# Kernel tuning notes

Hardware: AMD Instinct MI355X
Metric: run time of the kernel (lower is better)

Reference implementation:

```python
import math
import jax, jax.numpy as jnp
import numpy as np

B, S, E, H = 4, 1024, 768, 12
HD = E // H
NUM_BUCKETS, MAX_DIST = 320, 800


def setup_inputs() -> dict:
    key = jax.random.key(0)
    ks = jax.random.split(key, 8)
    w = lambda k, sh: jax.random.normal(k, sh, jnp.float32) * 0.02
    return {
        "hidden_states": jax.random.normal(ks[0], (B, S, E), jnp.float32),
        "q_w": w(ks[1], (E, E)), "q_b": jnp.zeros((E,), jnp.float32),
        "k_w": w(ks[2], (E, E)), "k_b": jnp.zeros((E,), jnp.float32),
        "v_w": w(ks[3], (E, E)), "v_b": jnp.zeros((E,), jnp.float32),
        "out_w": w(ks[4], (E, E)), "out_b": jnp.zeros((E,), jnp.float32),
        "gru_const": jnp.ones((1, H, 1, 1), jnp.float32),
        "gru_w": w(ks[5], (8, HD)), "gru_b": jnp.zeros((8,), jnp.float32),
        "rel_embed": w(ks[6], (NUM_BUCKETS, H)),
    }


def _relative_positions_bucket(rel):
    # rel: (S, S) int32, rel = memory_pos - context_pos
    nb = NUM_BUCKETS // 2
    buckets = (rel > 0).astype(jnp.int32) * nb
    rel = jnp.abs(rel)
    max_exact = nb // 2
    is_small = rel < max_exact
    large = jnp.log(rel.astype(jnp.float32) / max_exact)
    large = large / math.log(MAX_DIST / max_exact) * (nb - max_exact)
    large = (max_exact + large).astype(jnp.int32)
    large = jnp.minimum(large, nb - 1)
    return buckets + jnp.where(is_small, rel, large)


def _compute_position_bias(rel_embed):
    pos = jnp.arange(S, dtype=jnp.int32)
    rel = pos[None, :] - pos[:, None]              # (S, S)
    bucket = _relative_positions_bucket(rel)       # (S, S) int32
    return rel_embed[bucket].transpose(2, 0, 1)    # (H, S, S)


def reference(hidden_states, q_w, q_b, k_w, k_b, v_w, v_b, out_w, out_b,
              gru_const, gru_w, gru_b, rel_embed):
    position_bias = _compute_position_bias(rel_embed)          # (H, S, S)

    # gated relative-position bias
    ghs = hidden_states.reshape(B, S, H, HD).transpose(0, 2, 1, 3)   # (B,H,S,HD)
    proj = jnp.einsum("bhsd,ed->bhse", ghs, gru_w) + gru_b           # (B,H,S,8)
    proj = proj.reshape(B, H, S, 2, 4).sum(-1)                       # (B,H,S,2)
    gates = jax.nn.sigmoid(proj)
    gate_a, gate_b = gates[..., 0:1], gates[..., 1:2]                # (B,H,S,1)
    gate = gate_a * (gate_b * gru_const - 1.0) + 2.0                 # (B,H,S,1)
    gated_bias = gate[..., None, :, 0][..., None] * 0  # placeholder removed below
    gated_bias = gate * position_bias[None]                          # (B,H,S,S)

    scaling = HD ** -0.5
    q = (hidden_states @ q_w.T + q_b).reshape(B, S, H, HD).transpose(0, 2, 1, 3) * scaling
    k = (hidden_states @ k_w.T + k_b).reshape(B, S, H, HD).transpose(0, 2, 1, 3)
    v = (hidden_states @ v_w.T + v_b).reshape(B, S, H, HD).transpose(0, 2, 1, 3)

    scores = jnp.einsum("bhqd,bhkd->bhqk", q, k) + gated_bias
    attn = jax.nn.softmax(scores, axis=-1)
    ctx = jnp.einsum("bhqk,bhkd->bhqd", attn, v)                     # (B,H,S,HD)
    ctx = ctx.transpose(0, 2, 1, 3).reshape(B, S, E)
    attn_output = ctx @ out_w.T + out_b
    return attn_output, position_bias
```

## Files before the change

### kernel.cpp

```cpp
#include <hip/hip_runtime.h>

typedef unsigned short u16;
typedef __attribute__((ext_vector_type(4))) unsigned short u16x4;
typedef __attribute__((ext_vector_type(8))) short s8v;
typedef __attribute__((ext_vector_type(4))) float f4v;

#define BB 4
#define SS 1024
#define EE 768
#define HH 12
#define DD 64

#define NHS (BB * SS * EE)
#define NW  (EE * EE)
#define LOG2E 1.4426950408889634f

static __device__ __forceinline__ u16 f2bf(float x){
  unsigned int u = __float_as_uint(x);
  u += 0x7fffu + ((u >> 16) & 1u);
  return (u16)(u >> 16);
}
static __device__ __forceinline__ unsigned cvt_pk_bf16(float lo, float hi){
  unsigned r;
  asm("v_cvt_pk_bf16_f32 %0, %1, %2" : "=v"(r) : "v"(lo), "v"(hi));
  return r;
}
static __device__ __forceinline__ void stage16(const u16* g, u16* l){
  __builtin_amdgcn_global_load_lds(
      (const __attribute__((address_space(1))) void*)g,
      (__attribute__((address_space(3))) void*)l, 16, 0, 0);
}

__global__ __launch_bounds__(256) void prep_kernel(const float* __restrict__ hs,
                                                   const float* __restrict__ qw,
                                                   const float* __restrict__ kw,
                                                   const float* __restrict__ vw,
                                                   const float* __restrict__ ow,
                                                   u16* __restrict__ dst,
                                                   const float* __restrict__ rel_embed,
                                                   float* __restrict__ tbl,
                                                   const float* __restrict__ gru_w,
                                                   const float* __restrict__ gru_b,
                                                   const float* __restrict__ gru_c,
                                                   float* __restrict__ gate){
  const int bid = blockIdx.x;
  if (bid < 2688){
    size_t e = ((size_t)bid * 256 + threadIdx.x) * 8;
    const float* src;
    if      (e < (size_t)NHS)            src = hs + e;
    else if (e < (size_t)NHS + NW)       src = qw + (e - NHS);
    else if (e < (size_t)NHS + 2 * NW)   src = kw + (e - NHS - NW);
    else if (e < (size_t)NHS + 3 * NW)   src = vw + (e - NHS - 2 * (size_t)NW);
    else                                 src = ow + (e - NHS - 3 * (size_t)NW);
    f4v v0 = *(const f4v*)src, v1 = *(const f4v*)(src + 4);
    s8v o;
    #pragma unroll
    for (int i = 0; i < 4; i++){ o[i] = (short)f2bf(v0[i]); o[4 + i] = (short)f2bf(v1[i]); }
    size_t row = e / EE;
    int k = (int)(e - row * EE);
    size_t d = row * EE + (size_t)(k ^ (((int)row & 7) << 3));
    *(s8v*)(dst + d) = o;
  } else if (bid < 2784){
    int id = (bid - 2688) * 256 + threadIdx.x;
    int h = id >> 11, r = id & 2047;
    float v = 0.f;
    if (r < 2047){
      int rel = r - 1023;
      int bucket = (rel > 0) ? 160 : 0;
      int a = rel < 0 ? -rel : rel;
      int idx;
      if (a < 80) idx = a;
      else {
        float t = logf((float)a / 80.0f);
        t = t / 2.302585092994046f * 80.0f;
        int lg = (int)(80.0f + t);
        idx = lg < 159 ? lg : 159;
      }
      v = rel_embed[(idx + bucket) * HH + h];
    }
    tbl[id] = v;
  } else {
    int wid = (bid - 2784) * 4 + (threadIdx.x >> 6);
    int lane = threadIdx.x & 63;
    int s = wid & (SS - 1);
    int bh = wid >> 10;
    int h = bh % HH, b = bh / HH;
    float x = hs[(size_t)(b * SS + s) * EE + h * DD + lane];
    float w0 = gru_w[lane] + gru_w[64 + lane] + gru_w[128 + lane] + gru_w[192 + lane];
    float w1 = gru_w[256 + lane] + gru_w[320 + lane] + gru_w[384 + lane] + gru_w[448 + lane];
    float y0 = x * w0, y1 = x * w1;
    #pragma unroll
    for (int off = 1; off < 64; off <<= 1){
      y0 += __shfl_xor(y0, off);
      y1 += __shfl_xor(y1, off);
    }
    if (lane == 0){
      float s0 = y0 + gru_b[0] + gru_b[1] + gru_b[2] + gru_b[3];
      float s1 = y1 + gru_b[4] + gru_b[5] + gru_b[6] + gru_b[7];
      float ga = 1.f / (1.f + __expf(-s0));
      float gb = 1.f / (1.f + __expf(-s1));
      gate[wid] = ga * (gb * gru_c[h] - 1.0f) + 2.0f;
    }
  }
}

template<int EP>
static __device__ __forceinline__ void gemm_body(const u16* __restrict__ A,
                                                 const u16* __restrict__ Bw,
                                                 const float* __restrict__ bias,
                                                 void* __restrict__ Cp,
                                                 float scale, int m0, int n0){
  __shared__ __align__(16) u16 a_s[128 * 64];
  __shared__ __align__(16) u16 b_s[128 * 64];
  const int t = threadIdx.x;
  const int wave = t >> 6, lane = t & 63;
  const int lr = lane & 15, lg = lane >> 4;
  const int wm = (wave >> 1) * 64, wn = (wave & 1) * 64;
  const int srow = lane >> 3;
  const int scol = (lane & 7) * 8;
  const int swz = (lr & 7) << 3;

  const f4v zero = {0.f, 0.f, 0.f, 0.f};
  f4v acc[4][4];
  #pragma unroll
  for (int i = 0; i < 4; i++)
    #pragma unroll
    for (int j = 0; j < 4; j++) acc[i][j] = zero;

  for (int k0 = 0; k0 < EE; k0 += 64){
    if (k0) __syncthreads();
    #pragma unroll
    for (int i = 0; i < 4; i++){
      const int chunk = i * 4 + wave;
      const int r = chunk * 8 + srow;
      stage16(A  + (size_t)(m0 + r) * EE + k0 + scol, &a_s[chunk * 512]);
      stage16(Bw + (size_t)(n0 + r) * EE + k0 + scol, &b_s[chunk * 512]);
    }
    __syncthreads();
    #pragma unroll
    for (int kk = 0; kk < 2; kk++){
      const int cbase = (kk * 32 + lg * 8) ^ swz;
      s8v af[4], bf[4];
      #pragma unroll
      for (int i = 0; i < 4; i++){
        af[i] = *(const s8v*)&a_s[(wm + i * 16 + lr) * 64 + cbase];
        bf[i] = *(const s8v*)&b_s[(wn + i * 16 + lr) * 64 + cbase];
      }
      #pragma unroll
      for (int i = 0; i < 4; i++)
        #pragma unroll
        for (int j = 0; j < 4; j++)
          acc[i][j] = __builtin_amdgcn_mfma_f32_16x16x32_bf16(af[i], bf[j], acc[i][j], 0, 0, 0);
    }
  }

  #pragma unroll
  for (int ii = 0; ii < 4; ii++){
    const int row0 = m0 + wm + ii * 16 + lg * 4;
    const int bb = row0 >> 10;
    const int s0 = row0 & (SS - 1);
    #pragma unroll
    for (int j = 0; j < 4; j++){
      const int col = n0 + wn + j * 16 + lr;
      const float bv = bias[col];
      if (EP == 0){
        const int h = col >> 6, dim = col & 63;
        const int bh = bb * HH + h;
        u16* dst = (u16*)Cp + ((size_t)((bh * 64 + (s0 >> 4)) * 2 + (dim >> 5))) * 512
                   + ((dim >> 3) & 3) * 128 + (s0 & 15) * 8 + (dim & 7);
        #pragma unroll
        for (int r = 0; r < 4; r++)
          dst[r * 8] = f2bf((acc[ii][j][r] + bv) * scale);
      } else if (EP == 2){
        const int h = col >> 6, dim = col & 63;
        const int bh = bb * HH + h;
        u16x4 pk;
        #pragma unroll
        for (int r = 0; r < 4; r++) pk[r] = f2bf(acc[ii][j][r] + bv);
        *(u16x4*)((u16*)Cp + ((size_t)(((bh * 16 + (s0 >> 6)) * 2 + ((s0 >> 5) & 1)) * 4 + (dim >> 4))) * 512
                  + ((s0 >> 3) & 3) * 128 + (dim & 15) * 8 + (s0 & 7)) = pk;
      } else {
        #pragma unroll
        for (int r = 0; r < 4; r++)
          ((float*)Cp)[(size_t)(row0 + r) * EE + col] = acc[ii][j][r] + bv;
      }
    }
  }
}

__global__ __launch_bounds__(256) void gemm_qkv(const u16* __restrict__ A,
                                                const u16* __restrict__ wqkv,
                                                const float* __restrict__ bq,
                                                const float* __restrict__ bk,
                                                const float* __restrict__ bv,
                                                u16* __restrict__ qo,
                                                u16* __restrict__ ko,
                                                u16* __restrict__ vo){
  const int z = blockIdx.z;
  if (z == 2)
    gemm_body<2>(A, wqkv + 2 * (size_t)NW, bv, vo, 1.0f, blockIdx.x * 128, blockIdx.y * 128);
  else
    gemm_body<0>(A, wqkv + (size_t)z * NW, z ? bk : bq, z ? ko : qo,
                 z ? 1.0f : 0.125f * LOG2E, blockIdx.x * 128, blockIdx.y * 128);
}

__global__ __launch_bounds__(256) void gemm_out(const u16* __restrict__ A,
                                                const u16* __restrict__ Bw,
                                                const float* __restrict__ bias,
                                                float* __restrict__ Cp){
  gemm_body<1>(A, Bw, bias, Cp, 1.0f, blockIdx.x * 128, blockIdx.y * 128);
}

__global__ __launch_bounds__(256) void attn_kernel(const u16* __restrict__ qpack,
                                                   const u16* __restrict__ kpack,
                                                   const u16* __restrict__ vpack,
                                                   const float* __restrict__ gate,
                                                   const float* __restrict__ tbl,
                                                   u16* __restrict__ ctx,
                                                   float* __restrict__ pb){
  __shared__ __align__(16) float tbl_s[2048];
  __shared__ __align__(16) u16 kv_s[2][8192];
  __shared__ __align__(16) u16 p_s[4][16][72];
  const int t = threadIdx.x, wave = t >> 6, lane = t & 63;
  const int lr = lane & 15, lg = lane >> 4;
  const int i = blockIdx.x;
  const int xcd = i & 7, slot = i >> 3;
  const int bhg = xcd * 6 + (slot >> 4);
  const int qb  = slot & 15;
  const int b = bhg / HH, h = bhg % HH;
  const int bh = bhg;
  const int q0w = qb * 64 + wave * 16;
  {
    const float* th = tbl + h * 2048 + t * 8;
    *(f4v*)&tbl_s[t * 8]     = *(const f4v*)th;
    *(f4v*)&tbl_s[t * 8 + 4] = *(const f4v*)(th + 4);
  }
  const u16* qp = qpack + ((size_t)(bh * 64 + qb * 4 + wave)) * 1024 + lane * 8;
  const s8v qf0 = *(const s8v*)qp;
  const s8v qf1 = *(const s8v*)(qp + 512);
  const float gt = gate[(size_t)bh * SS + q0w + lr] * LOG2E;

  const u16* kbase = kpack + (size_t)bh * 65536;
  const u16* vbase = vpack + (size_t)bh * 65536;
  const int so = wave * 1024 + lane * 8;

  stage16(kbase + so,        &kv_s[0][wave * 1024]);
  stage16(kbase + so + 512,  &kv_s[0][wave * 1024 + 512]);
  stage16(vbase + so,        &kv_s[0][4096 + wave * 1024]);
  stage16(vbase + so + 512,  &kv_s[0][4096 + wave * 1024 + 512]);
  __syncthreads();

  const f4v zero = {0.f, 0.f, 0.f, 0.f};
  f4v o[4];
  #pragma unroll
  for (int d = 0; d < 4; d++) o[d] = zero;
  float l = 0.f;
  const int tb_off = 1023 - q0w + lg * 4 - lr;
  float* pbh = pb + (size_t)h * (SS * SS);
  const int i0 = (qb * 4 + b) * 16;

  for (int kt = 0; kt < 16; kt++){
    const int cur = kt & 1;
    if (kt < 15){
      const u16* kg = kbase + (kt + 1) * 4096;
      const u16* vg = vbase + (kt + 1) * 4096;
      u16* kl = &kv_s[cur ^ 1][wave * 1024];
      u16* vl = &kv_s[cur ^ 1][4096 + wave * 1024];
      stage16(kg + so,       kl);
      stage16(kg + so + 512, kl + 512);
      stage16(vg + so,       vl);
      stage16(vg + so + 512, vl + 512);
    }
    const u16* kl = &kv_s[cur][0];
    const u16* vl = &kv_s[cur][4096];
    s8v kf0[4], kf1[4];
    #pragma unroll
    for (int n = 0; n < 4; n++){
      kf0[n] = *(const s8v*)&kl[n * 1024 + lane * 8];
      kf1[n] = *(const s8v*)&kl[n * 1024 + 512 + lane * 8];
    }
    f4v sf[4];
    __builtin_amdgcn_s_setprio(1);
    #pragma unroll
    for (int n = 0; n < 4; n++){
      f4v z = zero;
      z = __builtin_amdgcn_mfma_f32_16x16x32_bf16(kf0[n], qf0, z, 0, 0, 0);
      z = __builtin_amdgcn_mfma_f32_16x16x32_bf16(kf1[n], qf1, z, 0, 0, 0);
      sf[n] = z;
    }
    __builtin_amdgcn_s_setprio(0);
    s8v vf0[4], vf1[4];
    #pragma unroll
    for (int d = 0; d < 4; d++){
      vf0[d] = *(const s8v*)&vl[d * 512 + lane * 8];
      vf1[d] = *(const s8v*)&vl[2048 + d * 512 + lane * 8];
    }
    float ps = 0.f;
    #pragma unroll
    for (int n = 0; n < 4; n++){
      const float* tp = &tbl_s[kt * 64 + n * 16 + tb_off];
      #pragma unroll
      for (int r = 0; r < 4; r++){
        float p = exp2f(sf[n][r] + gt * tp[r]);
        sf[n][r] = p;
        ps += p;
      }
    }
    l += ps;
    #pragma unroll
    for (int n = 0; n < 4; n++){
      unsigned pk0 = cvt_pk_bf16(sf[n][0], sf[n][1]);
      unsigned pk1 = cvt_pk_bf16(sf[n][2], sf[n][3]);
      u16* prow = &p_s[wave][lr][n * 16 + lg * 4];
      *(unsigned*)prow       = pk0;
      *(unsigned*)(prow + 2) = pk1;
    }
    const s8v pf0 = *(const s8v*)&p_s[wave][lr][lg * 8];
    const s8v pf1 = *(const s8v*)&p_s[wave][lr][32 + lg * 8];
    __builtin_amdgcn_s_setprio(1);
    #pragma unroll
    for (int d = 0; d < 4; d++){
      o[d] = __builtin_amdgcn_mfma_f32_16x16x32_bf16(pf0, vf0[d], o[d], 0, 0, 0);
      o[d] = __builtin_amdgcn_mfma_f32_16x16x32_bf16(pf1, vf1[d], o[d], 0, 0, 0);
    }
    __builtin_amdgcn_s_setprio(0);
    {
      const int ii = i0 + kt;
      const int base = 1023 - ii + t * 4;
      f4v v;
      v[0] = tbl_s[base + 0];
      v[1] = tbl_s[base + 1];
      v[2] = tbl_s[base + 2];
      v[3] = tbl_s[base + 3];
      __builtin_nontemporal_store(v, (f4v*)&pbh[(size_t)ii * SS + t * 4]);
    }
    __syncthreads();
  }
  l += __shfl_xor(l, 16);
  l += __shfl_xor(l, 32);
  float rl = 1.0f / l;
  float linv[4];
  #pragma unroll
  for (int r = 0; r < 4; r++) linv[r] = __shfl(rl, lg * 4 + r);
  #pragma unroll
  for (int d = 0; d < 4; d++)
    #pragma unroll
    for (int r = 0; r < 4; r++){
      float val = o[d][r] * linv[r];
      const int row = q0w + lg * 4 + r;
      const int col = (h * DD + d * 16 + lr) ^ ((row & 7) << 3);
      ctx[(size_t)(b * SS + row) * EE + col] = f2bf(val);
    }
}

extern "C" void kernel_launch(void* const* d_in, const int* in_sizes, int n_in,
                              void* d_out, int out_size, void* d_ws, size_t ws_size,
                              hipStream_t stream){
  const float* hs    = (const float*)d_in[0];
  const float* q_w   = (const float*)d_in[1];
  const float* q_b   = (const float*)d_in[2];
  const float* k_w   = (const float*)d_in[3];
  const float* k_b   = (const float*)d_in[4];
  const float* v_w   = (const float*)d_in[5];
  const float* v_b   = (const float*)d_in[6];
  const float* o_w   = (const float*)d_in[7];
  const float* o_b   = (const float*)d_in[8];
  const float* gru_c = (const float*)d_in[9];
  const float* gru_w = (const float*)d_in[10];
  const float* gru_b = (const float*)d_in[11];
  const float* rel   = (const float*)d_in[12];

  float* out0 = (float*)d_out;
  float* pb   = out0 + (size_t)BB * SS * EE;

  char* w = (char*)d_ws;
  u16* qpk  = (u16*)w;  w += (size_t)NHS * 2;
  u16* kpk  = (u16*)w;  w += (size_t)NHS * 2;
  u16* vpk  = (u16*)w;  w += (size_t)NHS * 2;
  u16* cvt  = (u16*)w;  w += ((size_t)NHS + 4 * (size_t)NW) * 2;
  float* gate = (float*)w; w += (size_t)BB * HH * SS * 4;
  float* tbl  = (float*)w;

  u16* hs_bf  = cvt;
  u16* wqkv   = cvt + NHS;
  u16* ow_bf  = cvt + NHS + 3 * (size_t)NW;

  prep_kernel<<<15072, 256, 0, stream>>>(hs, q_w, k_w, v_w, o_w, cvt,
                                         rel, tbl, gru_w, gru_b, gru_c, gate);
  gemm_qkv<<<dim3(32, 6, 3), 256, 0, stream>>>(hs_bf, wqkv, q_b, k_b, v_b, qpk, kpk, vpk);
  attn_kernel<<<768, 256, 0, stream>>>(qpk, kpk, vpk, gate, tbl, hs_bf, pb);
  gemm_out<<<dim3(32, 6), 256, 0, stream>>>(hs_bf, ow_bf, o_b, out0);
}
```

Baseline: 97.02 us.

## Load V fragments directly from global, triple-buffer K in LDS, defer bias stores

The attention kernel stops staging V through shared memory and instead loads V fragments straight from global memory into registers at the top of each key tile. K moves to a three-deep LDS ring with a prefetch distance of two tiles, and the full __syncthreads becomes a raw s_barrier plus sched_barrier fences, with the loop fully unrolled. Position-bias stores are moved out of the loop into a tail after the ctx write. The aim is to cut LDS traffic and barrier cost and keep the store stream off the critical path, at the cost of exposed global-load latency for V and more register pressure from unrolling. The s_barrier without a full wait on the async K staging may also be a correctness risk.

```diff
diff --git a/kernel.cpp b/kernel.cpp
--- a/kernel.cpp
+++ b/kernel.cpp
@@ -219,7 +219,7 @@
                                                    u16* __restrict__ ctx,
                                                    float* __restrict__ pb){
   __shared__ __align__(16) float tbl_s[2048];
-  __shared__ __align__(16) u16 kv_s[2][8192];
+  __shared__ __align__(16) u16 k_s[3][4096];
   __shared__ __align__(16) u16 p_s[4][16][72];
   const int t = threadIdx.x, wave = t >> 6, lane = t & 63;
   const int lr = lane & 15, lg = lane >> 4;
@@ -241,13 +241,13 @@
   const float gt = gate[(size_t)bh * SS + q0w + lr] * LOG2E;
 
   const u16* kbase = kpack + (size_t)bh * 65536;
-  const u16* vbase = vpack + (size_t)bh * 65536;
+  const u16* vp = vpack + (size_t)bh * 65536 + lane * 8;
   const int so = wave * 1024 + lane * 8;
 
-  stage16(kbase + so,        &kv_s[0][wave * 1024]);
-  stage16(kbase + so + 512,  &kv_s[0][wave * 1024 + 512]);
-  stage16(vbase + so,        &kv_s[0][4096 + wave * 1024]);
-  stage16(vbase + so + 512,  &kv_s[0][4096 + wave * 1024 + 512]);
+  stage16(kbase + so,               &k_s[0][wave * 1024]);
+  stage16(kbase + so + 512,         &k_s[0][wave * 1024 + 512]);
+  stage16(kbase + 4096 + so,        &k_s[1][wave * 1024]);
+  stage16(kbase + 4096 + so + 512,  &k_s[1][wave * 1024 + 512]);
   __syncthreads();
 
   const f4v zero = {0.f, 0.f, 0.f, 0.f};
@@ -259,20 +259,23 @@
   float* pbh = pb + (size_t)h * (SS * SS);
   const int i0 = (qb * 4 + b) * 16;
 
+  #pragma unroll
   for (int kt = 0; kt < 16; kt++){
-    const int cur = kt & 1;
-    if (kt < 15){
-      const u16* kg = kbase + (kt + 1) * 4096;
-      const u16* vg = vbase + (kt + 1) * 4096;
-      u16* kl = &kv_s[cur ^ 1][wave * 1024];
-      u16* vl = &kv_s[cur ^ 1][4096 + wave * 1024];
-      stage16(kg + so,       kl);
-      stage16(kg + so + 512, kl + 512);
-      stage16(vg + so,       vl);
-      stage16(vg + so + 512, vl + 512);
-    }
-    const u16* kl = &kv_s[cur][0];
-    const u16* vl = &kv_s[cur][4096];
+    s8v vf0[4], vf1[4];
+    #pragma unroll
+    for (int d = 0; d < 4; d++){
+      const u16* vr = vp + kt * 4096 + d * 512;
+      vf0[d] = *(const s8v*)vr;
+      vf1[d] = *(const s8v*)(vr + 2048);
+    }
+    __builtin_amdgcn_sched_barrier(0);
+    if (kt < 14){
+      const u16* kg = kbase + (kt + 2) * 4096;
+      u16* kd = &k_s[(kt + 2) % 3][wave * 1024];
+      stage16(kg + so,       kd);
+      stage16(kg + so + 512, kd + 512);
+    }
+    const u16* kl = &k_s[kt % 3][0];
     s8v kf0[4], kf1[4];
     #pragma unroll
     for (int n = 0; n < 4; n++){
@@ -289,12 +292,6 @@
       sf[n] = z;
     }
     __builtin_amdgcn_s_setprio(0);
-    s8v vf0[4], vf1[4];
-    #pragma unroll
-    for (int d = 0; d < 4; d++){
-      vf0[d] = *(const s8v*)&vl[d * 512 + lane * 8];
-      vf1[d] = *(const s8v*)&vl[2048 + d * 512 + lane * 8];
-    }
     float ps = 0.f;
     #pragma unroll
     for (int n = 0; n < 4; n++){
@@ -324,8 +321,28 @@
       o[d] = __builtin_amdgcn_mfma_f32_16x16x32_bf16(pf1, vf1[d], o[d], 0, 0, 0);
     }
     __builtin_amdgcn_s_setprio(0);
-    {
-      const int ii = i0 + kt;
+    __builtin_amdgcn_s_barrier();
+    __builtin_amdgcn_sched_barrier(0);
+  }
+  l += __shfl_xor(l, 16);
+  l += __shfl_xor(l, 32);
+  float rl = 1.0f / l;
+  float linv[4];
+  #pragma unroll
+  for (int r = 0; r < 4; r++) linv[r] = __shfl(rl, lg * 4 + r);
+  #pragma unroll
+  for (int d = 0; d < 4; d++)
+    #pragma unroll
+    for (int r = 0; r < 4; r++){
+      float val = o[d][r] * linv[r];
+      const int row = q0w + lg * 4 + r;
+      const int col = (h * DD + d * 16 + lr) ^ ((row & 7) << 3);
+      ctx[(size_t)(b * SS + row) * EE + col] = f2bf(val);
+    }
+  {
+    #pragma unroll 4
+    for (int rr = 0; rr < 16; rr++){
+      const int ii = i0 + rr;
       const int base = 1023 - ii + t * 4;
       f4v v;
       v[0] = tbl_s[base + 0];
@@ -334,23 +351,7 @@
       v[3] = tbl_s[base + 3];
       __builtin_nontemporal_store(v, (f4v*)&pbh[(size_t)ii * SS + t * 4]);
     }
-    __syncthreads();
-  }
-  l += __shfl_xor(l, 16);
-  l += __shfl_xor(l, 32);
-  float rl = 1.0f / l;
-  float linv[4];
-  #pragma unroll
-  for (int r = 0; r < 4; r++) linv[r] = __shfl(rl, lg * 4 + r);
-  #pragma unroll
-  for (int d = 0; d < 4; d++)
-    #pragma unroll
-    for (int r = 0; r < 4; r++){
-      float val = o[d][r] * linv[r];
-      const int row = q0w + lg * 4 + r;
-      const int col = (h * DD + d * 16 + lr) ^ ((row & 7) << 3);
-      ctx[(size_t)(b * SS + row) * EE + col] = f2bf(val);
-    }
+  }
 }
 
 extern "C" void kernel_launch(void* const* d_in, const int* in_sizes, int n_in,
```

Result: slower. 100.2 us (+3.3%).
